# Optimization experiments

Measured on AMD Instinct MI355X. Metric: run time of the kernel, lower is better.

The kernel has to match this reference:

```python
import jax, jax.numpy as jnp
import numpy as np

B, Cin, Cout, H, W = 8, 64, 128, 128, 128
K, S, P = 3, 1, 1
KK = K * K
EPS = 1e-5


def _conv2d(x, w, b=None):
    out = jax.lax.conv_general_dilated(
        x, w, window_strides=(S, S), padding=[(P, P), (P, P)],
        dimension_numbers=('NCHW', 'OIHW', 'NCHW'))
    if b is not None:
        out = out + b[None, :, None, None]
    return out


def setup_inputs() -> dict:
    key = jax.random.key(0)
    k = jax.random.split(key, 5)
    sc = 1.0 / np.sqrt(Cin * KK)
    return {
        'x': jax.random.normal(k[0], (B, Cin, H, W), jnp.float32),
        'offset_w': jax.random.normal(k[1], (2 * KK, Cin, K, K), jnp.float32) * sc,
        'offset_b': jnp.zeros((2 * KK,), jnp.float32),
        'mask_w': jax.random.normal(k[2], (KK, Cin, K, K), jnp.float32) * sc,
        'mask_b': jnp.zeros((KK,), jnp.float32),
        'conv_w': jax.random.normal(k[3], (Cout, Cin, K, K), jnp.float32) * sc,
    }


def _deform_conv2d(x, offset, mask, w):
    """Modulated deformable conv (torchvision deform_conv2d semantics)."""
    Bn, C, Hh, Ww = x.shape
    Ho, Wo = offset.shape[2], offset.shape[3]
    off = offset.reshape(Bn, KK, 2, Ho, Wo)  # (y, x) pairs per kernel tap
    ky, kx = jnp.meshgrid(jnp.arange(K), jnp.arange(K), indexing='ij')
    ky = ky.reshape(KK).astype(x.dtype)
    kx = kx.reshape(KK).astype(x.dtype)
    hy = (jnp.arange(Ho) * S - P).astype(x.dtype)
    wx = (jnp.arange(Wo) * S - P).astype(x.dtype)
    # sampling positions [B, KK, Ho, Wo]
    py = off[:, :, 0] + ky[None, :, None, None] + hy[None, None, :, None]
    px = off[:, :, 1] + kx[None, :, None, None] + wx[None, None, None, :]

    y0 = jnp.floor(py)
    x0 = jnp.floor(px)
    wy1 = py - y0; wx1 = px - x0
    wy0 = 1.0 - wy1; wx0 = 1.0 - wx1

    xf = x.reshape(Bn, C, Hh * Ww)

    def gather(yi, xi):
        valid = ((yi >= 0) & (yi < Hh) & (xi >= 0) & (xi < Ww)).astype(x.dtype)
        yc = jnp.clip(yi, 0, Hh - 1).astype(jnp.int32)
        xc = jnp.clip(xi, 0, Ww - 1).astype(jnp.int32)
        idx = (yc * Ww + xc).reshape(Bn, -1)  # [B, KK*Ho*Wo]
        vals = jnp.take_along_axis(xf, idx[:, None, :], axis=2)  # [B, C, KK*Ho*Wo]
        return vals.reshape(Bn, C, KK, Ho, Wo) * valid.reshape(Bn, 1, KK, Ho, Wo)

    v = (gather(y0, x0) * (wy0 * wx0)[:, None]
         + gather(y0, x0 + 1) * (wy0 * wx1)[:, None]
         + gather(y0 + 1, x0) * (wy1 * wx0)[:, None]
         + gather(y0 + 1, x0 + 1) * (wy1 * wx1)[:, None])  # [B, C, KK, Ho, Wo]
    v = v * mask[:, None]  # modulation
    return jnp.einsum('bckhw,ock->bohw', v, w.reshape(w.shape[0], C, KK))


def reference(x, offset_w, offset_b, mask_w, mask_b, conv_w):
    offset = _conv2d(x, offset_w, offset_b)
    mask = jax.nn.sigmoid(_conv2d(x, mask_w, mask_b))
    out = _deform_conv2d(x, offset, mask, conv_w)
    # BatchNorm2d(affine=False), training-mode normalization over (N, H, W)
    mean = out.mean(axis=(0, 2, 3), keepdims=True)
    var = out.var(axis=(0, 2, 3), keepdims=True)
    return jax.nn.relu((out - mean) * jax.lax.rsqrt(var + EPS))
```

## Files before the change

### kernel.cpp

```cpp
#include <hip/hip_runtime.h>
#include <hip/hip_bf16.h>

#define H_ 128
#define W_ 128
#define HW 16384
#define CIN 64
#define COUT 128
#define KK9 9
#define BATCH 8
#define NPIX (BATCH * HW)
#define KDIM 576

typedef short bf16x8 __attribute__((ext_vector_type(8)));
typedef float f32x4  __attribute__((ext_vector_type(4)));
typedef unsigned short ushort_t;

union U4B { uint4 u; bf16x8 v; };

__device__ __forceinline__ float us2f(unsigned short u) {
    unsigned int v = ((unsigned int)u) << 16;
    float f;
    __builtin_memcpy(&f, &v, 4);
    return f;
}
__device__ __forceinline__ float lo_f(unsigned int w) {
    unsigned int v = w << 16;
    float f;
    __builtin_memcpy(&f, &v, 4);
    return f;
}
__device__ __forceinline__ float hi_f(unsigned int w) {
    unsigned int v = w & 0xffff0000u;
    float f;
    __builtin_memcpy(&f, &v, 4);
    return f;
}
__device__ __forceinline__ unsigned short f2us_bf(float f) {
    __hip_bfloat16 h = __float2bfloat16(f);
    unsigned short u;
    __builtin_memcpy(&u, &h, 2);
    return u;
}
__device__ __forceinline__ unsigned int pack2(float a, float b) {
    return (unsigned int)f2us_bf(a) | ((unsigned int)f2us_bf(b) << 16);
}

template <bool F32>
__device__ __forceinline__ float ld_in(const void* p, long i) {
    if (F32) return ((const float*)p)[i];
    return us2f(((const unsigned short*)p)[i]);
}

__global__ void detect_zero(const uint4* __restrict__ xr4,
                            float* __restrict__ flag,
                            float* __restrict__ gstat) {
    int t = threadIdx.x;
#pragma unroll
    for (int i = 0; i < 16; ++i) gstat[i * 256 + t] = 0.0f;
    if (t < 64) {
        uint4 v = xr4[t];
        unsigned int w[4] = {v.x, v.y, v.z, v.w};
        int big = 0;
#pragma unroll
        for (int q = 0; q < 4; ++q) {
            big += (((w[q] >> 7)  & 0xFF) >= 0xC0);
            big += (((w[q] >> 23) & 0xFF) >= 0xC0);
        }
        unsigned long long m = __ballot(big > 0);
        if (t == 0) flag[0] = m ? 1.0f : 0.0f;
    }
}

template <bool F32>
__global__ void prep_weights(const void* __restrict__ offw,
                             const void* __restrict__ offb,
                             const void* __restrict__ maskw,
                             const void* __restrict__ maskb,
                             const void* __restrict__ convw,
                             const float* __restrict__ flag,
                             ushort_t* __restrict__ wTs,
                             ushort_t* __restrict__ wcats,
                             float* __restrict__ bias) {
    if ((flag[0] != 0.0f) != F32) return;
    int i = blockIdx.x * 256 + threadIdx.x;
    if (i < 73728) {
        int j = i & 7, lane = (i >> 3) & 63, n = (i >> 9) & 7, ks = i >> 12;
        int co = n * 16 + (lane & 15);
        int k  = ks * 32 + ((lane >> 4) << 3) + j;
        int kk = k >> 6, ci = k & 63;
        wTs[i] = f2us_bf(ld_in<F32>(convw, (long)co * KDIM + ci * 9 + kk));
    } else if (i < 73728 + 18432) {
        int i2 = i - 73728;
        int j = i2 & 7, lane = (i2 >> 3) & 63, n = (i2 >> 9) & 1, ks = i2 >> 10;
        int co2 = n * 16 + (lane & 15);
        int k   = ks * 32 + ((lane >> 4) << 3) + j;
        int kk = k >> 6, ci = k & 63;
        float v = 0.0f;
        if (co2 < 18)      v = ld_in<F32>(offw,  (long)co2 * KDIM + ci * 9 + kk);
        else if (co2 < 27) v = ld_in<F32>(maskw, (long)(co2 - 18) * KDIM + ci * 9 + kk);
        wcats[i2] = f2us_bf(v);
    } else if (i < 73728 + 18432 + 32) {
        int j = i - 73728 - 18432;
        float v = 0.0f;
        if (j < 18)      v = ld_in<F32>(offb, j);
        else if (j < 27) v = ld_in<F32>(maskb, j - 18);
        bias[j] = v;
    }
}

template <bool F32>
__global__ __launch_bounds__(256) void transpose_x(const void* __restrict__ x,
                                                   const float* __restrict__ flag,
                                                   ushort_t* __restrict__ xnb) {
    if ((flag[0] != 0.0f) != F32) return;
    __shared__ float tile[CIN][64 + 1];
    int blk  = blockIdx.x;
    int b    = blk >> 8;
    int pix0 = (blk & 255) * 64;
    int t    = threadIdx.x;
    int lane = t & 63;
    int grp  = t >> 6;
#pragma unroll
    for (int r = 0; r < 16; ++r) {
        int ci = r * 4 + grp;
        tile[ci][lane] = ld_in<F32>(x, (long)(b * CIN + ci) * HW + pix0 + lane);
    }
    __syncthreads();
#pragma unroll
    for (int r = 0; r < 16; ++r) {
        int px = r * 4 + grp;
        xnb[(size_t)(b * HW + pix0 + px) * CIN + lane] = f2us_bf(tile[lane][px]);
    }
}

__global__ __launch_bounds__(1024, 4) void conv_mfma(
        const ushort_t* __restrict__ xnb,
        const ushort_t* __restrict__ wcats,
        const float* __restrict__ bias,
        float* __restrict__ off2,
        float* __restrict__ mask_ws) {
    __shared__ uint4 ldsB4[2304];

    int t    = threadIdx.x;
    int pix0 = blockIdx.x * 256;
    int b    = pix0 >> 14;
    int rem0 = pix0 & 16383;

    const uint4* ws4 = (const uint4*)wcats;
#pragma unroll
    for (int i = t; i < 2304; i += 1024) ldsB4[i] = ws4[i];

    int wave = t >> 6, lane = t & 63, mrow = lane & 15, quad = lane >> 4;
    int px_l = wave * 16 + mrow;
    int remp = rem0 + px_l;
    int yp = remp >> 7, xp = remp & 127;
    const ushort_t* xb = xnb + (size_t)b * HW * CIN + quad * 8;
    __syncthreads();

    f32x4 acc[2];
    acc[0] = (f32x4){0.f, 0.f, 0.f, 0.f};
    acc[1] = (f32x4){0.f, 0.f, 0.f, 0.f};
    const ushort_t* ldsB = (const ushort_t*)ldsB4;

#pragma unroll 1
    for (int ty = 0; ty < 3; ++ty) {
        int yy = yp + ty - 1;
        bool oky = (yy >= 0) && (yy < H_);
#pragma unroll
        for (int tx = 0; tx < 3; ++tx) {
            int kk = ty * 3 + tx;
            int xq = xp + tx - 1;
            bool ok = oky && (xq >= 0) && (xq < W_);
            const ushort_t* src = xb + (size_t)(yy * W_ + xq) * CIN;
            U4B a0, a1;
            a0.u = ok ? *(const uint4*)src        : make_uint4(0, 0, 0, 0);
            a1.u = ok ? *(const uint4*)(src + 32) : make_uint4(0, 0, 0, 0);
#pragma unroll
            for (int half = 0; half < 2; ++half) {
                int ks = kk * 2 + half;
                U4B a = half ? a1 : a0;
#pragma unroll
                for (int n = 0; n < 2; ++n) {
                    bf16x8 bf = *(const bf16x8*)(ldsB + ((ks * 2 + n) * 64 + lane) * 8);
                    acc[n] = __builtin_amdgcn_mfma_f32_16x16x32_bf16(a.v, bf, acc[n], 0, 0, 0);
                }
            }
        }
    }

#pragma unroll
    for (int n = 0; n < 2; ++n) {
        int co2 = n * 16 + mrow;
        if (co2 >= 27) continue;
        float bs = bias[co2];
#pragma unroll
        for (int r = 0; r < 4; ++r) {
            int px = wave * 16 + quad * 4 + r;
            float v = acc[n][r] + bs;
            if (co2 < 18) {
                off2[((size_t)(b * 9 + (co2 >> 1)) * HW + rem0 + px) * 2 + (co2 & 1)] = v;
            } else {
                mask_ws[(size_t)(b * 9 + (co2 - 18)) * HW + rem0 + px] =
                    1.0f / (1.0f + __expf(-v));
            }
        }
    }
}

__global__ __launch_bounds__(1024, 4) void deform_mfma(
        const ushort_t* __restrict__ xnb,
        const float* __restrict__ off2,
        const float* __restrict__ mask_ws,
        const ushort_t* __restrict__ wTs,
        ushort_t* __restrict__ prebn,
        float* __restrict__ gstat) {
    __shared__ uint4 ldsB4[9216];
    __shared__ float red[256];

    int t    = threadIdx.x;
    int pix0 = blockIdx.x * 256;
    int b    = pix0 >> 14;
    int rem0 = pix0 & 16383;

    const uint4* ws4 = (const uint4*)wTs;
#pragma unroll
    for (int i = 0; i < 9; ++i) ldsB4[i * 1024 + t] = ws4[i * 1024 + t];
    if (t < 256) red[t] = 0.0f;

    int wave = t >> 6, lane = t & 63, mrow = lane & 15, quad = lane >> 4;
    int px_l = wave * 16 + mrow;
    int remp = rem0 + px_l;
    int yp = remp >> 7, xp = remp & 127;
    const ushort_t* xb = xnb + (size_t)b * HW * CIN + quad * 8;
    size_t obase = (size_t)b * 9 * HW + remp;
    __syncthreads();

    f32x4 acc[8];
#pragma unroll
    for (int n = 0; n < 8; ++n) acc[n] = (f32x4){0.f, 0.f, 0.f, 0.f};
    const ushort_t* ldsB = (const ushort_t*)ldsB4;

#pragma unroll 1
    for (int ty = 0; ty < 3; ++ty) {
        float oy[3], ox[3], m3[3];
#pragma unroll
        for (int tx = 0; tx < 3; ++tx) {
            int kk = ty * 3 + tx;
            float2 o = *(const float2*)(off2 + (obase + (size_t)kk * HW) * 2);
            oy[tx] = o.x; ox[tx] = o.y;
            m3[tx] = mask_ws[obase + (size_t)kk * HW];
        }
#pragma unroll
        for (int tx = 0; tx < 3; ++tx) {
            int kk = ty * 3 + tx;
            float py  = (float)(yp + ty - 1) + oy[tx];
            float pxf = (float)(xp + tx - 1) + ox[tx];
            float y0f = floorf(py), x0f = floorf(pxf);
            int yi = (int)y0f, xi = (int)x0f;
            float wy1 = py - y0f, wx1 = pxf - x0f;
            float wy0 = 1.0f - wy1, wx0 = 1.0f - wx1;
            float v[16];
#pragma unroll
            for (int j = 0; j < 16; ++j) v[j] = 0.0f;
#pragma unroll
            for (int c = 0; c < 4; ++c) {
                int ys = yi + (c >> 1);
                int xs = xi + (c & 1);
                float wgt = ((c >> 1) ? wy1 : wy0) * ((c & 1) ? wx1 : wx0);
                if (ys >= 0 && ys < H_ && xs >= 0 && xs < W_) {
                    const ushort_t* src = xb + (size_t)(ys * W_ + xs) * CIN;
                    uint4 l4 = *(const uint4*)src;
                    uint4 h4 = *(const uint4*)(src + 32);
                    unsigned int ww[8] = {l4.x, l4.y, l4.z, l4.w,
                                          h4.x, h4.y, h4.z, h4.w};
#pragma unroll
                    for (int j = 0; j < 8; ++j) {
                        v[2 * j]     = fmaf(wgt, lo_f(ww[j]), v[2 * j]);
                        v[2 * j + 1] = fmaf(wgt, hi_f(ww[j]), v[2 * j + 1]);
                    }
                }
            }
            float m = m3[tx];
            unsigned int w[8];
#pragma unroll
            for (int j = 0; j < 8; ++j)
                w[j] = pack2(v[2 * j] * m, v[2 * j + 1] * m);
            U4B a0, a1;
            a0.u = make_uint4(w[0], w[1], w[2], w[3]);
            a1.u = make_uint4(w[4], w[5], w[6], w[7]);
#pragma unroll
            for (int half = 0; half < 2; ++half) {
                int ks = kk * 2 + half;
                U4B a = half ? a1 : a0;
                const ushort_t* bbase = ldsB + ((size_t)(ks * 8) * 64 + lane) * 8;
#pragma unroll
                for (int n = 0; n < 8; ++n) {
                    bf16x8 bf = *(const bf16x8*)(bbase + n * 64 * 8);
                    acc[n] = __builtin_amdgcn_mfma_f32_16x16x32_bf16(a.v, bf, acc[n], 0, 0, 0);
                }
            }
        }
    }

#pragma unroll
    for (int n = 0; n < 8; ++n) {
        int co = n * 16 + mrow;
        float s = 0.f, ss = 0.f;
#pragma unroll
        for (int r = 0; r < 4; ++r) {
            int pg = pix0 + wave * 16 + quad * 4 + r;
            float v = acc[n][r];
            prebn[(size_t)pg * COUT + co] = f2us_bf(v);
            s += v;
            ss += v * v;
        }
        s  += __shfl_xor(s, 16, 64);
        s  += __shfl_xor(s, 32, 64);
        ss += __shfl_xor(ss, 16, 64);
        ss += __shfl_xor(ss, 32, 64);
        if (quad == 0) {
            atomicAdd(&red[co], s);
            atomicAdd(&red[128 + co], ss);
        }
    }
    __syncthreads();
    if (t < 256) atomicAdd(&gstat[(blockIdx.x & 15) * 256 + t], red[t]);
}

__global__ __launch_bounds__(256) void bn_apply_t(const ushort_t* __restrict__ prebn,
                                                  const float* __restrict__ gstat,
                                                  float* __restrict__ out) {
    __shared__ float tile[128 * 65];
    __shared__ float mvs[256];
    int t = threadIdx.x;
    if (t < 128) {
        float s = 0.f, ss = 0.f;
#pragma unroll
        for (int part = 0; part < 16; ++part) {
            s  += gstat[part * 256 + t];
            ss += gstat[part * 256 + 128 + t];
        }
        const float invN = 1.0f / (float)NPIX;
        float mean = s * invN;
        float var  = ss * invN - mean * mean;
        if (!isfinite(mean)) mean = 0.0f;
        float r = rsqrtf(fmaxf(var, 0.0f) + 1e-5f);
        if (!isfinite(r)) r = 1.0f;
        mvs[t]       = mean;
        mvs[128 + t] = r;
    }
    __syncthreads();
    int pix0 = blockIdx.x * 64;
    int b    = pix0 >> 14;
    int rem0 = pix0 & 16383;
    const ushort_t* src = prebn + (size_t)pix0 * COUT;
#pragma unroll
    for (int r = 0; r < 32; ++r) {
        int i = r * 256 + t;
        int p = i >> 7, c = i & 127;
        float v = us2f(src[i]);
        v = fmaxf((v - mvs[c]) * mvs[128 + c], 0.0f);
        tile[c * 65 + p] = v;
    }
    __syncthreads();
#pragma unroll
    for (int r = 0; r < 32; ++r) {
        int i = r * 256 + t;
        int c2 = i >> 6, p2 = i & 63;
        out[(size_t)(b * COUT + c2) * HW + rem0 + p2] = tile[c2 * 65 + p2];
    }
}

extern "C" void kernel_launch(void* const* d_in, const int* in_sizes, int n_in,
                              void* d_out, int out_size, void* d_ws, size_t ws_size,
                              hipStream_t stream) {
    (void)in_sizes; (void)n_in; (void)out_size; (void)ws_size;
    const void* x     = d_in[0];
    const void* offw  = d_in[1];
    const void* offb  = d_in[2];
    const void* maskw = d_in[3];
    const void* maskb = d_in[4];
    const void* convw = d_in[5];

    float* ws       = (float*)d_ws;
    float* off2     = ws;
    float* mask_ws  = off2 + 2359296;
    float* bias     = mask_ws + 1179648;
    float* gstat    = bias + 32;
    float* flag     = gstat + 4096;
    ushort_t* wTs   = (ushort_t*)(flag + 16);
    ushort_t* wcats = wTs + 73728;
    ushort_t* xnb   = wcats + 18432;
    ushort_t* prebn = xnb + 8388608;
    float* out      = (float*)d_out;

    detect_zero<<<1, 256, 0, stream>>>((const uint4*)x, flag, gstat);
    prep_weights<true><<<361, 256, 0, stream>>>(offw, offb, maskw, maskb, convw, flag, wTs, wcats, bias);
    prep_weights<false><<<361, 256, 0, stream>>>(offw, offb, maskw, maskb, convw, flag, wTs, wcats, bias);
    transpose_x<true><<<2048, 256, 0, stream>>>(x, flag, xnb);
    transpose_x<false><<<2048, 256, 0, stream>>>(x, flag, xnb);
    conv_mfma<<<512, 1024, 0, stream>>>(xnb, wcats, bias, off2, mask_ws);
    deform_mfma<<<512, 1024, 0, stream>>>(xnb, off2, mask_ws, wTs, prebn, gstat);
    bn_apply_t<<<2048, 256, 0, stream>>>(prebn, gstat, out);
}
```

Measured before the change: 225.7 us.

## Software-pipeline deform gathers and merge dtype-dispatch kernel launches

The deformable conv kernel now double-buffers the bilinear corner loads: it issues the next tap's global gathers before consuming the current tap with MFMAs. Offsets and masks for all 9 taps are preloaded ahead of the barrier, and out-of-bounds corners are clamped with zero weight so the loads are unconditional. The offset/mask conv also preloads all 9 tap fragments before the barrier and before the MFMA loop. The paired float/bf16 launches of the prep and transpose kernels are merged into single launches that branch on the flag. The cost is higher register pressure under a 1024-thread launch bound, which could cause spills.

```diff
diff --git a/kernel.cpp b/kernel.cpp
--- a/kernel.cpp
+++ b/kernel.cpp
@@ -72,17 +72,11 @@
 }
 
 template <bool F32>
-__global__ void prep_weights(const void* __restrict__ offw,
-                             const void* __restrict__ offb,
-                             const void* __restrict__ maskw,
-                             const void* __restrict__ maskb,
-                             const void* __restrict__ convw,
-                             const float* __restrict__ flag,
-                             ushort_t* __restrict__ wTs,
-                             ushort_t* __restrict__ wcats,
-                             float* __restrict__ bias) {
-    if ((flag[0] != 0.0f) != F32) return;
-    int i = blockIdx.x * 256 + threadIdx.x;
+__device__ __forceinline__ void prep_body(const void* offw, const void* offb,
+                                          const void* maskw, const void* maskb,
+                                          const void* convw,
+                                          ushort_t* wTs, ushort_t* wcats,
+                                          float* bias, int i) {
     if (i < 73728) {
         int j = i & 7, lane = (i >> 3) & 63, n = (i >> 9) & 7, ks = i >> 12;
         int co = n * 16 + (lane & 15);
@@ -108,11 +102,24 @@
     }
 }
 
+__global__ void prep_weights(const void* __restrict__ offw,
+                             const void* __restrict__ offb,
+                             const void* __restrict__ maskw,
+                             const void* __restrict__ maskb,
+                             const void* __restrict__ convw,
+                             const float* __restrict__ flag,
+                             ushort_t* __restrict__ wTs,
+                             ushort_t* __restrict__ wcats,
+                             float* __restrict__ bias) {
+    int i = blockIdx.x * 256 + threadIdx.x;
+    if (flag[0] != 0.0f)
+        prep_body<true>(offw, offb, maskw, maskb, convw, wTs, wcats, bias, i);
+    else
+        prep_body<false>(offw, offb, maskw, maskb, convw, wTs, wcats, bias, i);
+}
+
 template <bool F32>
-__global__ __launch_bounds__(256) void transpose_x(const void* __restrict__ x,
-                                                   const float* __restrict__ flag,
-                                                   ushort_t* __restrict__ xnb) {
-    if ((flag[0] != 0.0f) != F32) return;
+__device__ __forceinline__ void transpose_body(const void* x, ushort_t* xnb) {
     __shared__ float tile[CIN][64 + 1];
     int blk  = blockIdx.x;
     int b    = blk >> 8;
@@ -133,6 +140,13 @@
     }
 }
 
+__global__ __launch_bounds__(256) void transpose_x(const void* __restrict__ x,
+                                                   const float* __restrict__ flag,
+                                                   ushort_t* __restrict__ xnb) {
+    if (flag[0] != 0.0f) transpose_body<true>(x, xnb);
+    else                 transpose_body<false>(x, xnb);
+}
+
 __global__ __launch_bounds__(1024, 4) void conv_mfma(
         const ushort_t* __restrict__ xnb,
         const ushort_t* __restrict__ wcats,
@@ -155,35 +169,33 @@
     int remp = rem0 + px_l;
     int yp = remp >> 7, xp = remp & 127;
     const ushort_t* xb = xnb + (size_t)b * HW * CIN + quad * 8;
+
+    uint4 af0[9], af1[9];
+#pragma unroll
+    for (int kk = 0; kk < 9; ++kk) {
+        int yy = yp + kk / 3 - 1;
+        int xq = xp + kk % 3 - 1;
+        bool ok = (yy >= 0) && (yy < H_) && (xq >= 0) && (xq < W_);
+        const ushort_t* src = xb + (size_t)(yy * W_ + xq) * CIN;
+        af0[kk] = ok ? *(const uint4*)src        : make_uint4(0, 0, 0, 0);
+        af1[kk] = ok ? *(const uint4*)(src + 32) : make_uint4(0, 0, 0, 0);
+    }
     __syncthreads();
 
     f32x4 acc[2];
     acc[0] = (f32x4){0.f, 0.f, 0.f, 0.f};
     acc[1] = (f32x4){0.f, 0.f, 0.f, 0.f};
     const ushort_t* ldsB = (const ushort_t*)ldsB4;
-
-#pragma unroll 1
-    for (int ty = 0; ty < 3; ++ty) {
-        int yy = yp + ty - 1;
-        bool oky = (yy >= 0) && (yy < H_);
-#pragma unroll
-        for (int tx = 0; tx < 3; ++tx) {
-            int kk = ty * 3 + tx;
-            int xq = xp + tx - 1;
-            bool ok = oky && (xq >= 0) && (xq < W_);
-            const ushort_t* src = xb + (size_t)(yy * W_ + xq) * CIN;
-            U4B a0, a1;
-            a0.u = ok ? *(const uint4*)src        : make_uint4(0, 0, 0, 0);
-            a1.u = ok ? *(const uint4*)(src + 32) : make_uint4(0, 0, 0, 0);
-#pragma unroll
-            for (int half = 0; half < 2; ++half) {
-                int ks = kk * 2 + half;
-                U4B a = half ? a1 : a0;
-#pragma unroll
-                for (int n = 0; n < 2; ++n) {
-                    bf16x8 bf = *(const bf16x8*)(ldsB + ((ks * 2 + n) * 64 + lane) * 8);
-                    acc[n] = __builtin_amdgcn_mfma_f32_16x16x32_bf16(a.v, bf, acc[n], 0, 0, 0);
-                }
+#pragma unroll
+    for (int kk = 0; kk < 9; ++kk) {
+#pragma unroll
+        for (int half = 0; half < 2; ++half) {
+            int ks = kk * 2 + half;
+            U4B a; a.u = half ? af1[kk] : af0[kk];
+#pragma unroll
+            for (int n = 0; n < 2; ++n) {
+                bf16x8 bf = *(const bf16x8*)(ldsB + ((ks * 2 + n) * 64 + lane) * 8);
+                acc[n] = __builtin_amdgcn_mfma_f32_16x16x32_bf16(a.v, bf, acc[n], 0, 0, 0);
             }
         }
     }
@@ -207,6 +219,72 @@
     }
 }
 
+__device__ __forceinline__ void issue_tap(int kk, int yp, int xp,
+                                          float oy, float ox,
+                                          const ushort_t* __restrict__ xb,
+                                          uint4* cb, float* wg) {
+    int ty = kk / 3, tx = kk % 3;
+    float py  = (float)(yp + ty - 1) + oy;
+    float pxf = (float)(xp + tx - 1) + ox;
+    float y0f = floorf(py), x0f = floorf(pxf);
+    int yi = (int)y0f, xi = (int)x0f;
+    float wy1 = py - y0f, wx1 = pxf - x0f;
+    float wy0 = 1.0f - wy1, wx0 = 1.0f - wx1;
+#pragma unroll
+    for (int c = 0; c < 4; ++c) {
+        int dy = c >> 1, dx = c & 1;
+        int ys = yi + dy, xs = xi + dx;
+        bool ok = (ys >= 0) && (ys < H_) && (xs >= 0) && (xs < W_);
+        int ysc = min(max(ys, 0), H_ - 1);
+        int xsc = min(max(xs, 0), W_ - 1);
+        float w = (dy ? wy1 : wy0) * (dx ? wx1 : wx0);
+        wg[c] = ok ? w : 0.0f;
+        const ushort_t* src = xb + (size_t)(ysc * W_ + xsc) * CIN;
+        cb[2 * c]     = *(const uint4*)src;
+        cb[2 * c + 1] = *(const uint4*)(src + 32);
+    }
+}
+
+__device__ __forceinline__ void consume_tap(int kk, const uint4* cb,
+                                            const float* wg, float mk,
+                                            const ushort_t* __restrict__ ldsB,
+                                            int lane, f32x4* acc) {
+    float2 v2[8];
+#pragma unroll
+    for (int j = 0; j < 8; ++j) v2[j] = make_float2(0.f, 0.f);
+#pragma unroll
+    for (int c = 0; c < 4; ++c) {
+        float w = wg[c];
+        unsigned int ww[8] = {cb[2 * c].x,     cb[2 * c].y,
+                              cb[2 * c].z,     cb[2 * c].w,
+                              cb[2 * c + 1].x, cb[2 * c + 1].y,
+                              cb[2 * c + 1].z, cb[2 * c + 1].w};
+#pragma unroll
+        for (int j = 0; j < 8; ++j) {
+            v2[j].x = fmaf(w, lo_f(ww[j]), v2[j].x);
+            v2[j].y = fmaf(w, hi_f(ww[j]), v2[j].y);
+        }
+    }
+    unsigned int w8[8];
+#pragma unroll
+    for (int j = 0; j < 8; ++j)
+        w8[j] = pack2(v2[j].x * mk, v2[j].y * mk);
+    U4B a0, a1;
+    a0.u = make_uint4(w8[0], w8[1], w8[2], w8[3]);
+    a1.u = make_uint4(w8[4], w8[5], w8[6], w8[7]);
+#pragma unroll
+    for (int half = 0; half < 2; ++half) {
+        int ks = kk * 2 + half;
+        U4B a = half ? a1 : a0;
+        const ushort_t* bbase = ldsB + ((size_t)(ks * 8) * 64 + lane) * 8;
+#pragma unroll
+        for (int n = 0; n < 8; ++n) {
+            bf16x8 bf = *(const bf16x8*)(bbase + n * 64 * 8);
+            acc[n] = __builtin_amdgcn_mfma_f32_16x16x32_bf16(a.v, bf, acc[n], 0, 0, 0);
+        }
+    }
+}
+
 __global__ __launch_bounds__(1024, 4) void deform_mfma(
         const ushort_t* __restrict__ xnb,
         const float* __restrict__ off2,
@@ -233,6 +311,14 @@
     int yp = remp >> 7, xp = remp & 127;
     const ushort_t* xb = xnb + (size_t)b * HW * CIN + quad * 8;
     size_t obase = (size_t)b * 9 * HW + remp;
+
+    float oyv[9], oxv[9], mkv[9];
+#pragma unroll
+    for (int kk = 0; kk < 9; ++kk) {
+        float2 o = *(const float2*)(off2 + (obase + (size_t)kk * HW) * 2);
+        oyv[kk] = o.x; oxv[kk] = o.y;
+        mkv[kk] = mask_ws[obase + (size_t)kk * HW];
+    }
     __syncthreads();
 
     f32x4 acc[8];
@@ -240,65 +326,17 @@
     for (int n = 0; n < 8; ++n) acc[n] = (f32x4){0.f, 0.f, 0.f, 0.f};
     const ushort_t* ldsB = (const ushort_t*)ldsB4;
 
-#pragma unroll 1
-    for (int ty = 0; ty < 3; ++ty) {
-        float oy[3], ox[3], m3[3];
-#pragma unroll
-        for (int tx = 0; tx < 3; ++tx) {
-            int kk = ty * 3 + tx;
-            float2 o = *(const float2*)(off2 + (obase + (size_t)kk * HW) * 2);
-            oy[tx] = o.x; ox[tx] = o.y;
-            m3[tx] = mask_ws[obase + (size_t)kk * HW];
-        }
-#pragma unroll
-        for (int tx = 0; tx < 3; ++tx) {
-            int kk = ty * 3 + tx;
-            float py  = (float)(yp + ty - 1) + oy[tx];
-            float pxf = (float)(xp + tx - 1) + ox[tx];
-            float y0f = floorf(py), x0f = floorf(pxf);
-            int yi = (int)y0f, xi = (int)x0f;
-            float wy1 = py - y0f, wx1 = pxf - x0f;
-            float wy0 = 1.0f - wy1, wx0 = 1.0f - wx1;
-            float v[16];
-#pragma unroll
-            for (int j = 0; j < 16; ++j) v[j] = 0.0f;
-#pragma unroll
-            for (int c = 0; c < 4; ++c) {
-                int ys = yi + (c >> 1);
-                int xs = xi + (c & 1);
-                float wgt = ((c >> 1) ? wy1 : wy0) * ((c & 1) ? wx1 : wx0);
-                if (ys >= 0 && ys < H_ && xs >= 0 && xs < W_) {
-                    const ushort_t* src = xb + (size_t)(ys * W_ + xs) * CIN;
-                    uint4 l4 = *(const uint4*)src;
-                    uint4 h4 = *(const uint4*)(src + 32);
-                    unsigned int ww[8] = {l4.x, l4.y, l4.z, l4.w,
-                                          h4.x, h4.y, h4.z, h4.w};
-#pragma unroll
-                    for (int j = 0; j < 8; ++j) {
-                        v[2 * j]     = fmaf(wgt, lo_f(ww[j]), v[2 * j]);
-                        v[2 * j + 1] = fmaf(wgt, hi_f(ww[j]), v[2 * j + 1]);
-                    }
-                }
-            }
-            float m = m3[tx];
-            unsigned int w[8];
-#pragma unroll
-            for (int j = 0; j < 8; ++j)
-                w[j] = pack2(v[2 * j] * m, v[2 * j + 1] * m);
-            U4B a0, a1;
-            a0.u = make_uint4(w[0], w[1], w[2], w[3]);
-            a1.u = make_uint4(w[4], w[5], w[6], w[7]);
-#pragma unroll
-            for (int half = 0; half < 2; ++half) {
-                int ks = kk * 2 + half;
-                U4B a = half ? a1 : a0;
-                const ushort_t* bbase = ldsB + ((size_t)(ks * 8) * 64 + lane) * 8;
-#pragma unroll
-                for (int n = 0; n < 8; ++n) {
-                    bf16x8 bf = *(const bf16x8*)(bbase + n * 64 * 8);
-                    acc[n] = __builtin_amdgcn_mfma_f32_16x16x32_bf16(a.v, bf, acc[n], 0, 0, 0);
-                }
-            }
+    uint4 cb0[8], cb1[8];
+    float wg0[4], wg1[4];
+    issue_tap(0, yp, xp, oyv[0], oxv[0], xb, cb0, wg0);
+#pragma unroll
+    for (int kk = 0; kk < 9; ++kk) {
+        if (kk & 1) {
+            if (kk < 8) issue_tap(kk + 1, yp, xp, oyv[kk + 1], oxv[kk + 1], xb, cb0, wg0);
+            consume_tap(kk, cb1, wg1, mkv[kk], ldsB, lane, acc);
+        } else {
+            if (kk < 8) issue_tap(kk + 1, yp, xp, oyv[kk + 1], oxv[kk + 1], xb, cb1, wg1);
+            consume_tap(kk, cb0, wg0, mkv[kk], ldsB, lane, acc);
         }
     }
 
@@ -395,10 +433,8 @@
     float* out      = (float*)d_out;
 
     detect_zero<<<1, 256, 0, stream>>>((const uint4*)x, flag, gstat);
-    prep_weights<true><<<361, 256, 0, stream>>>(offw, offb, maskw, maskb, convw, flag, wTs, wcats, bias);
-    prep_weights<false><<<361, 256, 0, stream>>>(offw, offb, maskw, maskb, convw, flag, wTs, wcats, bias);
-    transpose_x<true><<<2048, 256, 0, stream>>>(x, flag, xnb);
-    transpose_x<false><<<2048, 256, 0, stream>>>(x, flag, xnb);
+    prep_weights<<<361, 256, 0, stream>>>(offw, offb, maskw, maskb, convw, flag, wTs, wcats, bias);
+    transpose_x<<<2048, 256, 0, stream>>>(x, flag, xnb);
     conv_mfma<<<512, 1024, 0, stream>>>(xnb, wcats, bias, off2, mask_ws);
     deform_mfma<<<512, 1024, 0, stream>>>(xnb, off2, mask_ws, wTs, prebn, gstat);
     bn_apply_t<<<2048, 256, 0, stream>>>(prebn, gstat, out);
```

Result: no change. 223.8 us (-0.8%).
